# Kernel optimization log

Measured on AMD Instinct MI355X. Metric: run time of the kernel, lower is better.

## Reference

```python
import jax, jax.numpy as jnp
import numpy as np

RATIO = 0.08  # self.ratio_3 (frozen parameter)
# kernel point k -> (dx, dy) = (k//3-1, k%3-1); matches torch.meshgrid('ij') flattening in offset_modulation
GX = np.repeat(np.arange(-1, 2), 3)  # [-1,-1,-1,0,0,0,1,1,1]
GY = np.tile(np.arange(-1, 2), 3)    # [-1,0,1,-1,0,1,-1,0,1]


def conv3(x, w, b):
    y = jax.lax.conv_general_dilated(x, w, (1, 1), ((1, 1), (1, 1)),
                                     dimension_numbers=('NCHW', 'OIHW', 'NCHW'))
    return y + b[None, :, None, None]


def offset_modulation(offset):
    B, C, H, W = offset.shape
    ov = offset.reshape(B, C // 2, 2, H, W)
    crop = ov[:, 3:12]                      # 9 (x,y) pairs
    oxy = jnp.concatenate([crop[:, :, 0], crop[:, :, 1]], axis=1) * RATIO  # [B,18,H,W]
    grid = jnp.concatenate([jnp.asarray(GX), jnp.asarray(GY)]).astype(offset.dtype)
    return oxy - grid[None, :, None, None]


def bilinear_sample(x, py, px):
    # x: [B,C,H,W]; py,px: [B,H,W] float sample coords; zero outside bounds
    B, C, H, W = x.shape
    y0 = jnp.floor(py); x0 = jnp.floor(px)
    wy = py - y0; wx = px - x0
    def gather(yi, xi):
        valid = ((yi >= 0) & (yi < H) & (xi >= 0) & (xi < W)).astype(x.dtype)
        yc = jnp.clip(yi, 0, H - 1).astype(jnp.int32)
        xc = jnp.clip(xi, 0, W - 1).astype(jnp.int32)
        g = jax.vmap(lambda img, yy, xx: img[:, yy, xx])(x, yc, xc)  # [B,C,H,W]
        return g * valid[:, None]
    return (gather(y0, x0) * ((1 - wy) * (1 - wx))[:, None]
            + gather(y0, x0 + 1) * ((1 - wy) * wx)[:, None]
            + gather(y0 + 1, x0) * (wy * (1 - wx))[:, None]
            + gather(y0 + 1, x0 + 1) * (wy * wx)[:, None])


def deform_conv(x, off, w, b):
    # off: [B,18,H,W], channels 0..8 = dx per kernel point, 9..17 = dy
    B, C, H, W = x.shape
    by = jnp.arange(H, dtype=x.dtype)[None, :, None]
    bx = jnp.arange(W, dtype=x.dtype)[None, None, :]
    out = jnp.zeros((B, w.shape[0], H, W), x.dtype)
    for k in range(9):
        py = by + GY[k] + off[:, 9 + k]
        px = bx + GX[k] + off[:, k]
        s = bilinear_sample(x, py, px)
        out = out + jnp.einsum('bchw,oc->bohw', s, w[:, :, GY[k] + 1, GX[k] + 1])
    return out + b[None, :, None, None]


def setup_inputs():
    key = jax.random.key(0)
    ks = iter(jax.random.split(key, 32))
    def p(*shape):
        return jax.random.normal(next(ks), shape, jnp.float32) * 0.05
    inp = {
        'x': jax.random.normal(next(ks), (2, 64, 256, 256), jnp.float32),
        'offset_0': jax.random.normal(next(ks), (2, 24, 256, 256), jnp.float32),
        'l12_w': p(64, 64, 3, 3), 'l12_b': p(64),
        'l13_w1': p(64, 64, 3, 3), 'l13_b1': p(64),
        'l13_w2': p(64, 64, 3, 3), 'l13_b2': p(64),
        'l14_w1': p(64, 64, 3, 3), 'l14_b1': p(64),
        'l14_w2': p(64, 64, 3, 3), 'l14_b2': p(64),
        'l15_w': p(32, 64, 3, 3), 'l15_b': p(32),
        'd50_w': p(32, 32, 3, 3), 'd50_b': p(32),
        'd51_w': p(32, 32, 3, 3), 'd51_b': p(32),
        'd60_w': p(32, 32, 3, 3), 'd60_b': p(32),
        'd61_w': p(32, 32, 3, 3), 'd61_b': p(32),
        'l24_w': p(3, 32, 3, 3), 'l24_b': p(3),
    }
    return inp


def reference(x, offset_0, l12_w, l12_b, l13_w1, l13_b1, l13_w2, l13_b2,
              l14_w1, l14_b1, l14_w2, l14_b2, l15_w, l15_b,
              d50_w, d50_b, d51_w, d51_b, d60_w, d60_b, d61_w, d61_b,
              l24_w, l24_b):
    off = offset_modulation(offset_0)
    x = conv3(x, l12_w, l12_b)
    x = conv3(jax.nn.relu(conv3(x, l13_w1, l13_b1)), l13_w2, l13_b2) + x
    x = conv3(jax.nn.relu(conv3(x, l14_w1, l14_b1)), l14_w2, l14_b2) + x
    x = conv3(x, l15_w, l15_b)
    r5 = jax.nn.relu(deform_conv(x, off, d50_w, d50_b))
    r5 = deform_conv(r5, off, d51_w, d51_b)
    x = x + r5
    r6 = jax.nn.relu(deform_conv(x, off, d60_w, d60_b))
    r6 = deform_conv(r6, off, d61_w, d61_b)
    x = x + r6
    return conv3(x, l24_w, l24_b)
```

## Files before the change

kernel.cpp:

```cpp
#include <hip/hip_runtime.h>

#define HH 256
#define WW 256
#define HW (HH * WW)

typedef float f32x4 __attribute__((ext_vector_type(4)));
typedef short bf16x8 __attribute__((ext_vector_type(8)));

__device__ __forceinline__ unsigned short f2bf(float f) {
    union { float f; unsigned u; } v; v.f = f;
    unsigned r = v.u + 0x7fff + ((v.u >> 16) & 1);
    return (unsigned short)(r >> 16);
}
__device__ __forceinline__ float bflo(unsigned u) {
    union { unsigned u; float f; } v; v.u = u << 16; return v.f;
}
__device__ __forceinline__ float bfhi(unsigned u) {
    union { unsigned u; float f; } v; v.u = u & 0xffff0000u; return v.f;
}
__device__ __forceinline__ unsigned cvtpk(float lo, float hi) {
    unsigned r;
    asm("v_cvt_pk_bf16_f32 %0, %1, %2" : "=v"(r) : "v"(lo), "v"(hi));
    return r;
}

__global__ void prepack_all(
    const float* w0, const float* w1, const float* w2, const float* w3,
    const float* w4, const float* w5, const float* w6, const float* w7,
    const float* w8, const float* w9,
    unsigned short* d0, unsigned short* d1, unsigned short* d2,
    unsigned short* d3, unsigned short* d4, unsigned short* d5,
    unsigned short* d6, unsigned short* d7, unsigned short* d8,
    unsigned short* d9) {
    const int L = blockIdx.y;
    const float* w; unsigned short* dst; int COUT, CIN;
    switch (L) {
        case 0: w = w0; dst = d0; COUT = 64; CIN = 64; break;
        case 1: w = w1; dst = d1; COUT = 64; CIN = 64; break;
        case 2: w = w2; dst = d2; COUT = 64; CIN = 64; break;
        case 3: w = w3; dst = d3; COUT = 64; CIN = 64; break;
        case 4: w = w4; dst = d4; COUT = 64; CIN = 64; break;
        case 5: w = w5; dst = d5; COUT = 32; CIN = 64; break;
        case 6: w = w6; dst = d6; COUT = 32; CIN = 32; break;
        case 7: w = w7; dst = d7; COUT = 32; CIN = 32; break;
        case 8: w = w8; dst = d8; COUT = 32; CIN = 32; break;
        default: w = w9; dst = d9; COUT = 32; CIN = 32; break;
    }
    int n = COUT * CIN * 9;
    int i = blockIdx.x * 256 + threadIdx.x;
    if (i >= n) return;
    int q = i & 31;
    int rest = i >> 5;
    int o = rest % COUT;
    int rest2 = rest / COUT;
    int KC = CIN >> 5;
    int kc = rest2 % KC;
    int t = rest2 / KC;
    int cin = kc * 32 + q;
    float v = w[((o * CIN + cin) * 3 + t / 3) * 3 + (t % 3)];
    dst[i] = f2bf(v);
}

template <bool SRCF32, int CIN, int COUT, bool RELU, bool ADDRES>
__global__ __launch_bounds__((COUT / 32) * 128) void convmfma(
    const void* __restrict__ in_, const unsigned short* __restrict__ wp,
    const float* __restrict__ bias, const unsigned short* __restrict__ res,
    unsigned short* __restrict__ out) {
    constexpr int KC = CIN / 32;
    constexpr int WM = COUT / 32;
    constexpr int NT = WM * 128;
    constexpr int CSTR = (CIN == 64) ? 72 : 40;
    __shared__ unsigned short xt[204 * CSTR];

    const int tid = threadIdx.x;
    const int b = blockIdx.z;
    const int bx0 = blockIdx.x * 32;
    const int by0 = blockIdx.y * 4;

    if (SRCF32) {
        const float* inb = (const float*)in_ + (size_t)b * CIN * HW;
        for (int hp = tid; hp < 204; hp += NT) {
            int hy = hp / 34, hx = hp - hy * 34;
            int gy = by0 + hy - 1, gx = bx0 + hx - 1;
            bool ok = ((unsigned)gy < HH) && ((unsigned)gx < WW);
            const float* src = inb + ((size_t)gy * WW + gx);
            unsigned* dstp = (unsigned*)&xt[hp * CSTR];
#pragma unroll 4
            for (int c = 0; c < CIN; c += 2) {
                float v0 = ok ? src[(size_t)c * HW] : 0.f;
                float v1 = ok ? src[(size_t)(c + 1) * HW] : 0.f;
                dstp[c >> 1] = cvtpk(v0, v1);
            }
        }
    } else {
        const unsigned short* inb = (const unsigned short*)in_ + (size_t)b * HW * CIN;
        constexpr int CH = CIN / 8;
        for (int idx = tid; idx < 204 * CH; idx += NT) {
            int hp = idx / CH, sub = idx - hp * CH;
            int hy = hp / 34, hx = hp - hy * 34;
            int gy = by0 + hy - 1, gx = bx0 + hx - 1;
            uint4 v = {0, 0, 0, 0};
            if (((unsigned)gy < HH) && ((unsigned)gx < WW))
                v = *(const uint4*)&inb[((size_t)gy * WW + gx) * CIN + sub * 8];
            *(uint4*)&xt[hp * CSTR + sub * 8] = v;
        }
    }
    __syncthreads();

    const int lane = tid & 63;
    const int wv = tid >> 6;
    const int wm = (WM == 2) ? (wv & 1) : 0;
    const int wn = (WM == 2) ? (wv >> 1) : wv;
    const int l15 = lane & 15;
    const int kg = lane >> 4;

    f32x4 acc[2][4];
#pragma unroll
    for (int m = 0; m < 2; ++m)
#pragma unroll
        for (int n = 0; n < 4; ++n) acc[m][n] = {0.f, 0.f, 0.f, 0.f};

    int hbase[4];
#pragma unroll
    for (int n = 0; n < 4; ++n) {
        int p = wn * 64 + n * 16 + l15;
        hbase[n] = (p >> 5) * 34 + (p & 31);
    }

    const unsigned short* wlane = wp + ((size_t)(wm * 32 + l15) * 4 + kg) * 8;

#pragma unroll
    for (int t = 0; t < 9; ++t) {
        bf16x8 afr[2][KC];
#pragma unroll
        for (int kc = 0; kc < KC; ++kc)
#pragma unroll
            for (int m = 0; m < 2; ++m)
                afr[m][kc] = *(const bf16x8*)(wlane + ((size_t)(t * KC + kc) * COUT + m * 16) * 32);

        const int hoff = (t / 3) * 34 + (t % 3);
#pragma unroll
        for (int kc = 0; kc < KC; ++kc) {
            bf16x8 bfr[4];
#pragma unroll
            for (int n = 0; n < 4; ++n)
                bfr[n] = *(const bf16x8*)&xt[(hbase[n] + hoff) * CSTR + kc * 32 + kg * 8];
#pragma unroll
            for (int m = 0; m < 2; ++m)
#pragma unroll
                for (int n = 0; n < 4; ++n)
                    acc[m][n] = __builtin_amdgcn_mfma_f32_16x16x32_bf16(afr[m][kc], bfr[n], acc[m][n], 0, 0, 0);
        }
    }

    const size_t pixbase = (size_t)b * HW;
#pragma unroll
    for (int m = 0; m < 2; ++m) {
#pragma unroll
        for (int n = 0; n < 4; ++n) {
            int p = wn * 64 + n * 16 + l15;
            int gy = by0 + (p >> 5), gx = bx0 + (p & 31);
            size_t pidx = (pixbase + (size_t)gy * WW + gx) * COUT;
            int cb = wm * 32 + m * 16 + kg * 4;
            float v[4];
#pragma unroll
            for (int r = 0; r < 4; ++r) {
                v[r] = acc[m][n][r] + bias[cb + r];
                if (RELU) v[r] = fmaxf(v[r], 0.f);
            }
            if (ADDRES) {
                uint2 rr = *(const uint2*)&res[pidx + cb];
                v[0] += bflo(rr.x); v[1] += bfhi(rr.x);
                v[2] += bflo(rr.y); v[3] += bfhi(rr.y);
            }
            uint2 o;
            o.x = cvtpk(v[0], v[1]);
            o.y = cvtpk(v[2], v[3]);
            *(uint2*)&out[pidx + cb] = o;
        }
    }
}

__global__ __launch_bounds__(512) void dpair(
    const unsigned short* __restrict__ in, const float* __restrict__ off0,
    const unsigned short* __restrict__ w1p, const float* __restrict__ b1,
    const unsigned short* __restrict__ w2p, const float* __restrict__ b2,
    unsigned short* __restrict__ out) {
    constexpr int CS = 40;
    constexpr int MIDB = 432 * CS;
    __shared__ unsigned short xt[(432 + 352) * CS];

    const int tid = threadIdx.x;
    const int b = blockIdx.z;
    const int bx0 = blockIdx.x * 32;
    const int by0 = blockIdx.y * 8;

    const unsigned short* inb = in + (size_t)b * HW * 32;
    for (int idx = tid; idx < 432 * 4; idx += 512) {
        int hp = idx >> 2, sub = idx & 3;
        int hy = hp / 36, hx = hp - hy * 36;
        int gy = by0 + hy - 2, gx = bx0 + hx - 2;
        uint4 v = {0, 0, 0, 0};
        if (((unsigned)gy < HH) && ((unsigned)gx < WW))
            v = *(const uint4*)&inb[((size_t)gy * WW + gx) * 32 + sub * 8];
        *(uint4*)&xt[hp * CS + sub * 8] = v;
    }
    __syncthreads();

    const int lane = tid & 63;
    const int wv = tid >> 6;
    const int l15 = lane & 15;
    const int kg = lane >> 4;
    const float* offB = off0 + (size_t)b * 24 * HW;

    f32x4 acc1[2][3];
#pragma unroll
    for (int m = 0; m < 2; ++m)
#pragma unroll
        for (int f = 0; f < 3; ++f) acc1[m][f] = {0.f, 0.f, 0.f, 0.f};

    int fgy[3], fgx[3], foff[3];
#pragma unroll
    for (int f = 0; f < 3; ++f) {
        int id = (wv * 3 + f) * 16 + l15;
        int rid = min(id, 339);
        int iy = rid / 34, ix = rid - iy * 34;
        fgy[f] = by0 - 1 + iy;
        fgx[f] = bx0 - 1 + ix;
        int cy = min(max(fgy[f], 0), HH - 1);
        int cx = min(max(fgx[f], 0), WW - 1);
        foff[f] = cy * WW + cx;
    }
    const unsigned short* w1l = w1p + (size_t)(l15 * 32 + kg * 8);

#pragma unroll 1
    for (int t = 0; t < 9; ++t) {
        const int k = (t % 3) * 3 + t / 3;
        const float* offx = offB + (size_t)(6 + 2 * k) * HW;
        const float* offy = offB + (size_t)(7 + 2 * k) * HW;
        bf16x8 afr[2];
#pragma unroll
        for (int m = 0; m < 2; ++m)
            afr[m] = *(const bf16x8*)(w1l + (size_t)(t * 32 + m * 16) * 32);

        bf16x8 bfr[3];
#pragma unroll
        for (int f = 0; f < 3; ++f) {
            float dxv = offx[foff[f]] * 0.08f;
            float dyv = offy[foff[f]] * 0.08f;
            float pxf = (float)fgx[f] + dxv;
            float pyf = (float)fgy[f] + dyv;
            float x0f = floorf(pxf), y0f = floorf(pyf);
            float wx = pxf - x0f, wy = pyf - y0f;
            int tx0 = min(max((int)x0f - (bx0 - 2), 0), 34);
            int ty0 = min(max((int)y0f - (by0 - 2), 0), 10);
            int lp = ty0 * 36 + tx0;
            uint4 a00 = *(const uint4*)&xt[lp * CS + kg * 8];
            uint4 a01 = *(const uint4*)&xt[(lp + 1) * CS + kg * 8];
            uint4 a10 = *(const uint4*)&xt[(lp + 36) * CS + kg * 8];
            uint4 a11 = *(const uint4*)&xt[(lp + 37) * CS + kg * 8];
            float w00 = (1.f - wy) * (1.f - wx), w01 = (1.f - wy) * wx;
            float w10 = wy * (1.f - wx), w11 = wy * wx;
            unsigned c00[4] = {a00.x, a00.y, a00.z, a00.w};
            unsigned c01[4] = {a01.x, a01.y, a01.z, a01.w};
            unsigned c10[4] = {a10.x, a10.y, a10.z, a10.w};
            unsigned c11[4] = {a11.x, a11.y, a11.z, a11.w};
            union { bf16x8 v; unsigned u[4]; } ur;
#pragma unroll
            for (int j = 0; j < 4; ++j) {
                float slo = w00 * bflo(c00[j]);
                slo = fmaf(w01, bflo(c01[j]), slo);
                slo = fmaf(w10, bflo(c10[j]), slo);
                slo = fmaf(w11, bflo(c11[j]), slo);
                float shi = w00 * bfhi(c00[j]);
                shi = fmaf(w01, bfhi(c01[j]), shi);
                shi = fmaf(w10, bfhi(c10[j]), shi);
                shi = fmaf(w11, bfhi(c11[j]), shi);
                ur.u[j] = cvtpk(slo, shi);
            }
            bfr[f] = ur.v;
        }
#pragma unroll
        for (int m = 0; m < 2; ++m)
#pragma unroll
            for (int f = 0; f < 3; ++f)
                acc1[m][f] = __builtin_amdgcn_mfma_f32_16x16x32_bf16(afr[m], bfr[f], acc1[m][f], 0, 0, 0);
    }
#pragma unroll
    for (int f = 0; f < 3; ++f) {
        int id = (wv * 3 + f) * 16 + l15;
        bool ok = ((unsigned)fgy[f] < HH) && ((unsigned)fgx[f] < WW) && (id < 340);
        int wid = min(id, 351);
#pragma unroll
        for (int m = 0; m < 2; ++m) {
            int cb = m * 16 + kg * 4;
            float v[4];
#pragma unroll
            for (int r = 0; r < 4; ++r)
                v[r] = ok ? fmaxf(acc1[m][f][r] + b1[cb + r], 0.f) : 0.f;
            uint2 o;
            o.x = cvtpk(v[0], v[1]);
            o.y = cvtpk(v[2], v[3]);
            *(uint2*)&xt[MIDB + wid * CS + cb] = o;
        }
    }
    __syncthreads();

    f32x4 acc2[2][2];
#pragma unroll
    for (int m = 0; m < 2; ++m)
#pragma unroll
        for (int n = 0; n < 2; ++n) acc2[m][n] = {0.f, 0.f, 0.f, 0.f};

    const int py = by0 + wv;
    const unsigned short* w2l = w2p + (size_t)(l15 * 32 + kg * 8);

#pragma unroll 1
    for (int t = 0; t < 9; ++t) {
        const int k = (t % 3) * 3 + t / 3;
        const float* offx = offB + (size_t)(6 + 2 * k) * HW + (size_t)py * WW;
        const float* offy = offB + (size_t)(7 + 2 * k) * HW + (size_t)py * WW;
        bf16x8 afr[2];
#pragma unroll
        for (int m = 0; m < 2; ++m)
            afr[m] = *(const bf16x8*)(w2l + (size_t)(t * 32 + m * 16) * 32);

        bf16x8 bfr[2];
#pragma unroll
        for (int n = 0; n < 2; ++n) {
            const int pxi = bx0 + n * 16 + l15;
            float dxv = offx[pxi] * 0.08f;
            float dyv = offy[pxi] * 0.08f;
            float pxf = (float)pxi + dxv;
            float pyf = (float)py + dyv;
            float x0f = floorf(pxf), y0f = floorf(pyf);
            float wx = pxf - x0f, wy = pyf - y0f;
            int mx0 = min(max((int)x0f - (bx0 - 1), 0), 32);
            int my0 = min(max((int)y0f - (by0 - 1), 0), 8);
            int lp = my0 * 34 + mx0;
            uint4 a00 = *(const uint4*)&xt[MIDB + lp * CS + kg * 8];
            uint4 a01 = *(const uint4*)&xt[MIDB + (lp + 1) * CS + kg * 8];
            uint4 a10 = *(const uint4*)&xt[MIDB + (lp + 34) * CS + kg * 8];
            uint4 a11 = *(const uint4*)&xt[MIDB + (lp + 35) * CS + kg * 8];
            float w00 = (1.f - wy) * (1.f - wx), w01 = (1.f - wy) * wx;
            float w10 = wy * (1.f - wx), w11 = wy * wx;
            unsigned c00[4] = {a00.x, a00.y, a00.z, a00.w};
            unsigned c01[4] = {a01.x, a01.y, a01.z, a01.w};
            unsigned c10[4] = {a10.x, a10.y, a10.z, a10.w};
            unsigned c11[4] = {a11.x, a11.y, a11.z, a11.w};
            union { bf16x8 v; unsigned u[4]; } ur;
#pragma unroll
            for (int j = 0; j < 4; ++j) {
                float slo = w00 * bflo(c00[j]);
                slo = fmaf(w01, bflo(c01[j]), slo);
                slo = fmaf(w10, bflo(c10[j]), slo);
                slo = fmaf(w11, bflo(c11[j]), slo);
                float shi = w00 * bfhi(c00[j]);
                shi = fmaf(w01, bfhi(c01[j]), shi);
                shi = fmaf(w10, bfhi(c10[j]), shi);
                shi = fmaf(w11, bfhi(c11[j]), shi);
                ur.u[j] = cvtpk(slo, shi);
            }
            bfr[n] = ur.v;
        }
#pragma unroll
        for (int m = 0; m < 2; ++m)
#pragma unroll
            for (int n = 0; n < 2; ++n)
                acc2[m][n] = __builtin_amdgcn_mfma_f32_16x16x32_bf16(afr[m], bfr[n], acc2[m][n], 0, 0, 0);
    }

    unsigned short* outb = out + (size_t)b * HW * 32;
#pragma unroll
    for (int n = 0; n < 2; ++n) {
        int gx = bx0 + n * 16 + l15;
        int rs = (wv + 2) * 36 + (n * 16 + l15) + 2;
        size_t pidx = ((size_t)py * WW + gx) * 32;
#pragma unroll
        for (int m = 0; m < 2; ++m) {
            int cb = m * 16 + kg * 4;
            float v[4];
#pragma unroll
            for (int r = 0; r < 4; ++r) v[r] = acc2[m][n][r] + b2[cb + r];
            uint2 rr = *(const uint2*)&xt[rs * CS + cb];
            v[0] += bflo(rr.x); v[1] += bfhi(rr.x);
            v[2] += bflo(rr.y); v[3] += bfhi(rr.y);
            uint2 o;
            o.x = cvtpk(v[0], v[1]);
            o.y = cvtpk(v[2], v[3]);
            *(uint2*)&outb[pidx + cb] = o;
        }
    }
}

__global__ __launch_bounds__(256) void conv3f(const unsigned short* __restrict__ in,
                                              const float* __restrict__ wgt,
                                              const float* __restrict__ bias,
                                              float* __restrict__ out) {
    __shared__ unsigned short xt[324 * 34];
    const int tid = threadIdx.x;
    const int lx = tid & 15, ly = tid >> 4;
    const int bx = blockIdx.x << 4, by = blockIdx.y << 4;
    const int b = blockIdx.z;

    const unsigned short* inb = in + (size_t)b * HW * 32;
    for (int idx = tid; idx < 324 * 8; idx += 256) {
        int hp = idx >> 3, sub = idx & 7;
        int hy = hp / 18, hx = hp - hy * 18;
        int gy = by + hy - 1, gx = bx + hx - 1;
        uint2 v = {0, 0};
        if (((unsigned)gy < HH) && ((unsigned)gx < WW))
            v = *(const uint2*)&inb[((size_t)gy * WW + gx) * 32 + sub * 4];
        *(uint2*)&xt[hp * 34 + sub * 4] = v;
    }
    __syncthreads();

    float a0 = bias[0], a1 = bias[1], a2 = bias[2];
#pragma unroll
    for (int ty = 0; ty < 3; ++ty) {
#pragma unroll
        for (int tx = 0; tx < 3; ++tx) {
            const unsigned short* row = &xt[((ly + ty) * 18 + lx + tx) * 34];
#pragma unroll 8
            for (int c = 0; c < 32; c += 2) {
                unsigned pv = *(const unsigned*)&row[c];
                float vl = bflo(pv), vh = bfhi(pv);
                const float* wl = wgt + (size_t)(c * 3 + ty) * 3 + tx;
                const float* whp = wgt + (size_t)((c + 1) * 3 + ty) * 3 + tx;
                a0 = fmaf(vl, wl[0], a0);          a0 = fmaf(vh, whp[0], a0);
                a1 = fmaf(vl, wl[32 * 9], a1);     a1 = fmaf(vh, whp[32 * 9], a1);
                a2 = fmaf(vl, wl[64 * 9], a2);     a2 = fmaf(vh, whp[64 * 9], a2);
            }
        }
    }
    const size_t o0 = ((size_t)b * 3) * HW + (size_t)(by + ly) * WW + bx + lx;
    out[o0] = a0;
    out[o0 + HW] = a1;
    out[o0 + 2 * HW] = a2;
}

extern "C" void kernel_launch(void* const* d_in, const int* in_sizes, int n_in,
                              void* d_out, int out_size, void* d_ws, size_t ws_size,
                              hipStream_t stream) {
    const float* x    = (const float*)d_in[0];
    const float* off0 = (const float*)d_in[1];
    const float* w12  = (const float*)d_in[2];
    const float* b12  = (const float*)d_in[3];
    const float* w13a = (const float*)d_in[4];
    const float* b13a = (const float*)d_in[5];
    const float* w13b = (const float*)d_in[6];
    const float* b13b = (const float*)d_in[7];
    const float* w14a = (const float*)d_in[8];
    const float* b14a = (const float*)d_in[9];
    const float* w14b = (const float*)d_in[10];
    const float* b14b = (const float*)d_in[11];
    const float* w15  = (const float*)d_in[12];
    const float* b15  = (const float*)d_in[13];
    const float* w50  = (const float*)d_in[14];
    const float* b50  = (const float*)d_in[15];
    const float* w51  = (const float*)d_in[16];
    const float* b51  = (const float*)d_in[17];
    const float* w60  = (const float*)d_in[18];
    const float* b60  = (const float*)d_in[19];
    const float* w61  = (const float*)d_in[20];
    const float* b61  = (const float*)d_in[21];
    const float* w24  = (const float*)d_in[22];
    const float* b24  = (const float*)d_in[23];

    unsigned short* A  = (unsigned short*)d_ws;
    unsigned short* Bb = A + (size_t)2 * HW * 64;
    unsigned short* D  = Bb;
    unsigned short* E  = Bb + (size_t)2 * HW * 32;
    unsigned short* wpk = Bb + (size_t)2 * HW * 64;
    const int SZ64 = 64 * 64 * 9;
    const int SZ32 = 32 * 64 * 9;
    const int SZD  = 32 * 32 * 9;
    unsigned short* p12  = wpk;
    unsigned short* p13a = p12 + SZ64;
    unsigned short* p13b = p13a + SZ64;
    unsigned short* p14a = p13b + SZ64;
    unsigned short* p14b = p14a + SZ64;
    unsigned short* p15  = p14b + SZ64;
    unsigned short* q50  = p15 + SZ32;
    unsigned short* q51  = q50 + SZD;
    unsigned short* q60  = q51 + SZD;
    unsigned short* q61  = q60 + SZD;
    float* out = (float*)d_out;

    prepack_all<<<dim3(144, 10), 256, 0, stream>>>(
        w12, w13a, w13b, w14a, w14b, w15, w50, w51, w60, w61,
        p12, p13a, p13b, p14a, p14b, p15, q50, q51, q60, q61);

    dim3 gm(WW / 32, HH / 4, 2);
    dim3 gd(WW / 32, HH / 8, 2);
    dim3 gs(HH / 16, WW / 16, 2);

    convmfma<true,  64, 64, false, false><<<gm, 256, 0, stream>>>(x,  p12,  b12,  nullptr, A);
    convmfma<false, 64, 64, true,  false><<<gm, 256, 0, stream>>>(A,  p13a, b13a, nullptr, Bb);
    convmfma<false, 64, 64, false, true ><<<gm, 256, 0, stream>>>(Bb, p13b, b13b, A, A);
    convmfma<false, 64, 64, true,  false><<<gm, 256, 0, stream>>>(A,  p14a, b14a, nullptr, Bb);
    convmfma<false, 64, 64, false, true ><<<gm, 256, 0, stream>>>(Bb, p14b, b14b, A, A);
    convmfma<false, 64, 32, false, false><<<gm, 128, 0, stream>>>(A,  p15,  b15,  nullptr, D);

    dpair<<<gd, 512, 0, stream>>>(D, off0, q50, b50, q51, b51, E);
    dpair<<<gd, 512, 0, stream>>>(E, off0, q60, b60, q61, b61, D);
    conv3f<<<gs, 256, 0, stream>>>(D, w24, b24, out);
}
```

Measured before the change: 217.2 us.

## Shrink deformable pair tile to 4 rows, reuse LDS, pack bilinear FMAs

The fused deformable-conv pair kernel now processes a 32x4 output tile instead of 32x8. It reuses one shared buffer for both the input halo and the intermediate activations, with an extra barrier in between, so the shared-memory footprint drops sharply and occupancy can rise. The residual is now read from global memory instead of from shared memory. Bilinear interpolation is factored into a helper that uses packed v_pk_mul/v_pk_fma f32 instructions. The smaller tile recomputes a proportionally larger halo of first-stage outputs (204 vs 340 positions for half the outputs), adding redundant work.

```diff
diff --git a/kernel.cpp b/kernel.cpp
--- a/kernel.cpp
+++ b/kernel.cpp
@@ -5,6 +5,7 @@
 #define HW (HH * WW)
 
 typedef float f32x4 __attribute__((ext_vector_type(4)));
+typedef float f32x2 __attribute__((ext_vector_type(2)));
 typedef short bf16x8 __attribute__((ext_vector_type(8)));
 
 __device__ __forceinline__ unsigned short f2bf(float f) {
@@ -22,6 +23,50 @@
     unsigned r;
     asm("v_cvt_pk_bf16_f32 %0, %1, %2" : "=v"(r) : "v"(lo), "v"(hi));
     return r;
+}
+__device__ __forceinline__ f32x2 pkmul(f32x2 a, f32x2 b) {
+    f32x2 d;
+    asm("v_pk_mul_f32 %0, %1, %2" : "=v"(d) : "v"(a), "v"(b));
+    return d;
+}
+__device__ __forceinline__ f32x2 pkfma(f32x2 a, f32x2 b, f32x2 c) {
+    f32x2 d;
+    asm("v_pk_fma_f32 %0, %1, %2, %3" : "=v"(d) : "v"(a), "v"(b), "v"(c));
+    return d;
+}
+__device__ __forceinline__ f32x2 up2(unsigned u) {
+    f32x2 r; 
+    union { unsigned u; float f; } lo, hi;
+    lo.u = u << 16; hi.u = u & 0xffff0000u;
+    r[0] = lo.f; r[1] = hi.f;
+    return r;
+}
+
+template <int W>
+__device__ __forceinline__ bf16x8 lerp8(const unsigned short* __restrict__ tile,
+                                        int lp, float wx, float wy, int kg) {
+    const unsigned short* p = tile + lp * 40 + kg * 8;
+    uint4 a00 = *(const uint4*)p;
+    uint4 a01 = *(const uint4*)(p + 40);
+    uint4 a10 = *(const uint4*)(p + W * 40);
+    uint4 a11 = *(const uint4*)(p + W * 40 + 40);
+    float omx = 1.f - wx, omy = 1.f - wy;
+    float s00 = omy * omx, s01 = omy * wx, s10 = wy * omx, s11 = wy * wx;
+    f32x2 w00p = {s00, s00}, w01p = {s01, s01}, w10p = {s10, s10}, w11p = {s11, s11};
+    unsigned c00[4] = {a00.x, a00.y, a00.z, a00.w};
+    unsigned c01[4] = {a01.x, a01.y, a01.z, a01.w};
+    unsigned c10[4] = {a10.x, a10.y, a10.z, a10.w};
+    unsigned c11[4] = {a11.x, a11.y, a11.z, a11.w};
+    union { bf16x8 v; unsigned u[4]; } ur;
+#pragma unroll
+    for (int j = 0; j < 4; ++j) {
+        f32x2 s = pkmul(w00p, up2(c00[j]));
+        s = pkfma(w01p, up2(c01[j]), s);
+        s = pkfma(w10p, up2(c10[j]), s);
+        s = pkfma(w11p, up2(c11[j]), s);
+        ur.u[j] = cvtpk(s[0], s[1]);
+    }
+    return ur.v;
 }
 
 __global__ void prepack_all(
@@ -187,16 +232,15 @@
     const unsigned short* __restrict__ w2p, const float* __restrict__ b2,
     unsigned short* __restrict__ out) {
     constexpr int CS = 40;
-    constexpr int MIDB = 432 * CS;
-    __shared__ unsigned short xt[(432 + 352) * CS];
+    __shared__ unsigned short xt[288 * CS];
 
     const int tid = threadIdx.x;
     const int b = blockIdx.z;
     const int bx0 = blockIdx.x * 32;
-    const int by0 = blockIdx.y * 8;
+    const int by0 = blockIdx.y * 4;
 
     const unsigned short* inb = in + (size_t)b * HW * 32;
-    for (int idx = tid; idx < 432 * 4; idx += 512) {
+    for (int idx = tid; idx < 288 * 4; idx += 512) {
         int hp = idx >> 2, sub = idx & 3;
         int hy = hp / 36, hx = hp - hy * 36;
         int gy = by0 + hy - 2, gx = bx0 + hx - 2;
@@ -213,17 +257,17 @@
     const int kg = lane >> 4;
     const float* offB = off0 + (size_t)b * 24 * HW;
 
-    f32x4 acc1[2][3];
+    f32x4 acc1[2][2];
 #pragma unroll
     for (int m = 0; m < 2; ++m)
 #pragma unroll
-        for (int f = 0; f < 3; ++f) acc1[m][f] = {0.f, 0.f, 0.f, 0.f};
-
-    int fgy[3], fgx[3], foff[3];
-#pragma unroll
-    for (int f = 0; f < 3; ++f) {
-        int id = (wv * 3 + f) * 16 + l15;
-        int rid = min(id, 339);
+        for (int f = 0; f < 2; ++f) acc1[m][f] = {0.f, 0.f, 0.f, 0.f};
+
+    int fgy[2], fgx[2], foff[2];
+#pragma unroll
+    for (int f = 0; f < 2; ++f) {
+        int id = (wv * 2 + f) * 16 + l15;
+        int rid = min(id, 203);
         int iy = rid / 34, ix = rid - iy * 34;
         fgy[f] = by0 - 1 + iy;
         fgx[f] = bx0 - 1 + ix;
@@ -243,9 +287,9 @@
         for (int m = 0; m < 2; ++m)
             afr[m] = *(const bf16x8*)(w1l + (size_t)(t * 32 + m * 16) * 32);
 
-        bf16x8 bfr[3];
-#pragma unroll
-        for (int f = 0; f < 3; ++f) {
+#pragma unroll
+        for (int f = 0; f < 2; ++f) {
+            if ((wv * 2 + f) * 16 >= 204) continue;
             float dxv = offx[foff[f]] * 0.08f;
             float dyv = offy[foff[f]] * 0.08f;
             float pxf = (float)fgx[f] + dxv;
@@ -253,44 +297,19 @@
             float x0f = floorf(pxf), y0f = floorf(pyf);
             float wx = pxf - x0f, wy = pyf - y0f;
             int tx0 = min(max((int)x0f - (bx0 - 2), 0), 34);
-            int ty0 = min(max((int)y0f - (by0 - 2), 0), 10);
-            int lp = ty0 * 36 + tx0;
-            uint4 a00 = *(const uint4*)&xt[lp * CS + kg * 8];
-            uint4 a01 = *(const uint4*)&xt[(lp + 1) * CS + kg * 8];
-            uint4 a10 = *(const uint4*)&xt[(lp + 36) * CS + kg * 8];
-            uint4 a11 = *(const uint4*)&xt[(lp + 37) * CS + kg * 8];
-            float w00 = (1.f - wy) * (1.f - wx), w01 = (1.f - wy) * wx;
-            float w10 = wy * (1.f - wx), w11 = wy * wx;
-            unsigned c00[4] = {a00.x, a00.y, a00.z, a00.w};
-            unsigned c01[4] = {a01.x, a01.y, a01.z, a01.w};
-            unsigned c10[4] = {a10.x, a10.y, a10.z, a10.w};
-            unsigned c11[4] = {a11.x, a11.y, a11.z, a11.w};
-            union { bf16x8 v; unsigned u[4]; } ur;
-#pragma unroll
-            for (int j = 0; j < 4; ++j) {
-                float slo = w00 * bflo(c00[j]);
-                slo = fmaf(w01, bflo(c01[j]), slo);
-                slo = fmaf(w10, bflo(c10[j]), slo);
-                slo = fmaf(w11, bflo(c11[j]), slo);
-                float shi = w00 * bfhi(c00[j]);
-                shi = fmaf(w01, bfhi(c01[j]), shi);
-                shi = fmaf(w10, bfhi(c10[j]), shi);
-                shi = fmaf(w11, bfhi(c11[j]), shi);
-                ur.u[j] = cvtpk(slo, shi);
-            }
-            bfr[f] = ur.v;
-        }
-#pragma unroll
-        for (int m = 0; m < 2; ++m)
-#pragma unroll
-            for (int f = 0; f < 3; ++f)
-                acc1[m][f] = __builtin_amdgcn_mfma_f32_16x16x32_bf16(afr[m], bfr[f], acc1[m][f], 0, 0, 0);
-    }
-#pragma unroll
-    for (int f = 0; f < 3; ++f) {
-        int id = (wv * 3 + f) * 16 + l15;
-        bool ok = ((unsigned)fgy[f] < HH) && ((unsigned)fgx[f] < WW) && (id < 340);
-        int wid = min(id, 351);
+            int ty0 = min(max((int)y0f - (by0 - 2), 0), 6);
+            bf16x8 bfr = lerp8<36>(xt, ty0 * 36 + tx0, wx, wy, kg);
+#pragma unroll
+            for (int m = 0; m < 2; ++m)
+                acc1[m][f] = __builtin_amdgcn_mfma_f32_16x16x32_bf16(afr[m], bfr, acc1[m][f], 0, 0, 0);
+        }
+    }
+    __syncthreads();
+
+#pragma unroll
+    for (int f = 0; f < 2; ++f) {
+        int id = (wv * 2 + f) * 16 + l15;
+        bool ok = ((unsigned)fgy[f] < HH) && ((unsigned)fgx[f] < WW) && (id < 204);
 #pragma unroll
         for (int m = 0; m < 2; ++m) {
             int cb = m * 16 + kg * 4;
@@ -301,18 +320,17 @@
             uint2 o;
             o.x = cvtpk(v[0], v[1]);
             o.y = cvtpk(v[2], v[3]);
-            *(uint2*)&xt[MIDB + wid * CS + cb] = o;
+            *(uint2*)&xt[id * CS + cb] = o;
         }
     }
     __syncthreads();
 
-    f32x4 acc2[2][2];
-#pragma unroll
-    for (int m = 0; m < 2; ++m)
-#pragma unroll
-        for (int n = 0; n < 2; ++n) acc2[m][n] = {0.f, 0.f, 0.f, 0.f};
-
-    const int py = by0 + wv;
+    f32x4 acc2[2];
+#pragma unroll
+    for (int m = 0; m < 2; ++m) acc2[m] = {0.f, 0.f, 0.f, 0.f};
+
+    const int py = by0 + (wv >> 1);
+    const int pxb = bx0 + (wv & 1) * 16;
     const unsigned short* w2l = w2p + (size_t)(l15 * 32 + kg * 8);
 
 #pragma unroll 1
@@ -325,71 +343,37 @@
         for (int m = 0; m < 2; ++m)
             afr[m] = *(const bf16x8*)(w2l + (size_t)(t * 32 + m * 16) * 32);
 
-        bf16x8 bfr[2];
-#pragma unroll
-        for (int n = 0; n < 2; ++n) {
-            const int pxi = bx0 + n * 16 + l15;
-            float dxv = offx[pxi] * 0.08f;
-            float dyv = offy[pxi] * 0.08f;
-            float pxf = (float)pxi + dxv;
-            float pyf = (float)py + dyv;
-            float x0f = floorf(pxf), y0f = floorf(pyf);
-            float wx = pxf - x0f, wy = pyf - y0f;
-            int mx0 = min(max((int)x0f - (bx0 - 1), 0), 32);
-            int my0 = min(max((int)y0f - (by0 - 1), 0), 8);
-            int lp = my0 * 34 + mx0;
-            uint4 a00 = *(const uint4*)&xt[MIDB + lp * CS + kg * 8];
-            uint4 a01 = *(const uint4*)&xt[MIDB + (lp + 1) * CS + kg * 8];
-            uint4 a10 = *(const uint4*)&xt[MIDB + (lp + 34) * CS + kg * 8];
-            uint4 a11 = *(const uint4*)&xt[MIDB + (lp + 35) * CS + kg * 8];
-            float w00 = (1.f - wy) * (1.f - wx), w01 = (1.f - wy) * wx;
-            float w10 = wy * (1.f - wx), w11 = wy * wx;
-            unsigned c00[4] = {a00.x, a00.y, a00.z, a00.w};
-            unsigned c01[4] = {a01.x, a01.y, a01.z, a01.w};
-            unsigned c10[4] = {a10.x, a10.y, a10.z, a10.w};
-            unsigned c11[4] = {a11.x, a11.y, a11.z, a11.w};
-            union { bf16x8 v; unsigned u[4]; } ur;
-#pragma unroll
-            for (int j = 0; j < 4; ++j) {
-                float slo = w00 * bflo(c00[j]);
-                slo = fmaf(w01, bflo(c01[j]), slo);
-                slo = fmaf(w10, bflo(c10[j]), slo);
-                slo = fmaf(w11, bflo(c11[j]), slo);
-                float shi = w00 * bfhi(c00[j]);
-                shi = fmaf(w01, bfhi(c01[j]), shi);
-                shi = fmaf(w10, bfhi(c10[j]), shi);
-                shi = fmaf(w11, bfhi(c11[j]), shi);
-                ur.u[j] = cvtpk(slo, shi);
-            }
-            bfr[n] = ur.v;
-        }
+        const int pxi = pxb + l15;
+        float dxv = offx[pxi] * 0.08f;
+        float dyv = offy[pxi] * 0.08f;
+        float pxf = (float)pxi + dxv;
+        float pyf = (float)py + dyv;
+        float x0f = floorf(pxf), y0f = floorf(pyf);
+        float wx = pxf - x0f, wy = pyf - y0f;
+        int mx0 = min(max((int)x0f - (bx0 - 1), 0), 32);
+        int my0 = min(max((int)y0f - (by0 - 1), 0), 4);
+        bf16x8 bfr = lerp8<34>(xt, my0 * 34 + mx0, wx, wy, kg);
 #pragma unroll
         for (int m = 0; m < 2; ++m)
-#pragma unroll
-            for (int n = 0; n < 2; ++n)
-                acc2[m][n] = __builtin_amdgcn_mfma_f32_16x16x32_bf16(afr[m], bfr[n], acc2[m][n], 0, 0, 0);
-    }
-
+            acc2[m] = __builtin_amdgcn_mfma_f32_16x16x32_bf16(afr[m], bfr, acc2[m], 0, 0, 0);
+    }
+
+    const int gx = pxb + l15;
+    const size_t pidx = ((size_t)py * WW + gx) * 32;
     unsigned short* outb = out + (size_t)b * HW * 32;
 #pragma unroll
-    for (int n = 0; n < 2; ++n) {
-        int gx = bx0 + n * 16 + l15;
-        int rs = (wv + 2) * 36 + (n * 16 + l15) + 2;
-        size_t pidx = ((size_t)py * WW + gx) * 32;
-#pragma unroll
-        for (int m = 0; m < 2; ++m) {
-            int cb = m * 16 + kg * 4;
-            float v[4];
-#pragma unroll
-            for (int r = 0; r < 4; ++r) v[r] = acc2[m][n][r] + b2[cb + r];
-            uint2 rr = *(const uint2*)&xt[rs * CS + cb];
-            v[0] += bflo(rr.x); v[1] += bfhi(rr.x);
-            v[2] += bflo(rr.y); v[3] += bfhi(rr.y);
-            uint2 o;
-            o.x = cvtpk(v[0], v[1]);
-            o.y = cvtpk(v[2], v[3]);
-            *(uint2*)&outb[pidx + cb] = o;
-        }
+    for (int m = 0; m < 2; ++m) {
+        int cb = m * 16 + kg * 4;
+        float v[4];
+#pragma unroll
+        for (int r = 0; r < 4; ++r) v[r] = acc2[m][r] + b2[cb + r];
+        uint2 rr = *(const uint2*)&inb[pidx + cb];
+        v[0] += bflo(rr.x); v[1] += bfhi(rr.x);
+        v[2] += bflo(rr.y); v[3] += bfhi(rr.y);
+        uint2 o;
+        o.x = cvtpk(v[0], v[1]);
+        o.y = cvtpk(v[2], v[3]);
+        *(uint2*)&outb[pidx + cb] = o;
     }
 }
 
@@ -492,7 +476,7 @@
         p12, p13a, p13b, p14a, p14b, p15, q50, q51, q60, q61);
 
     dim3 gm(WW / 32, HH / 4, 2);
-    dim3 gd(WW / 32, HH / 8, 2);
+    dim3 gd(WW / 32, HH / 4, 2);
     dim3 gs(HH / 16, WW / 16, 2);
 
     convmfma<true,  64, 64, false, false><<<gm, 256, 0, stream>>>(x,  p12,  b12,  nullptr, A);
```

Result: slower. 236.5 us (+8.9%).
